# Performance work log

Measured on AMD Instinct MI355X. Metric: run time of the kernel, lower is better.

The kernel has to match this reference:

```python
import jax, jax.numpy as jnp
import numpy as np

B, M_IN, M_OUT, C = 4, 16, 32, 32


def setup_inputs() -> dict:
    key = jax.random.key(0)
    kx, = jax.random.split(key, 1)
    x = jax.random.normal(kx, (B, M_IN, C, C, C, C), dtype=jnp.float32)
    init = jnp.ones((M_IN, M_OUT), dtype=jnp.float32) / M_IN
    return {"x": x, "alpha": init, "beta": init, "gamma": init, "delta": init}


def reference(x, alpha, beta, gamma, delta):
    # Faithful to the torch code's permute+sum bookkeeping (note: torch's
    # permute(0,1,3,2,4,5).sum((2,4,5)) reduces ORIGINAL axes (3,4,5),
    # keeping original axis 2 -- identical to s1).
    s1 = x.sum(axis=(3, 4, 5))  # (B, M_in, C), keeps axis 2
    s2 = x.sum(axis=(3, 4, 5))  # same as s1 (permuted-sum in torch keeps axis 2)
    s3 = x.sum(axis=(2, 4, 5))  # keeps axis 3
    s4 = x.sum(axis=(2, 3, 5))  # keeps axis 4
    s = jnp.stack([s1, s2, s3, s4], axis=2)            # (B, M_in, 4, C)
    w = jnp.stack([alpha, beta, gamma, delta], axis=2)  # (M_in, M_out, 4)
    # 'bmic,mnd->bnic': sums over m and w's stack axis d; keeps s's stack axis i.
    out = jnp.einsum('bmic,mnd->bnic', s, w)            # (B, M_out, 4, C)
    return out
```

## Files before the change

kernel.cpp:

```cpp
#include <hip/hip_runtime.h>


__global__ __launch_bounds__(256) void zero_k(float* __restrict__ ws) {
    int i = blockIdx.x * 256 + threadIdx.x;
    if (i < 6144) ws[i] = 0.0f;
}

__global__ __launch_bounds__(256) void reduce_k(const float* __restrict__ x,
                                                float* __restrict__ ws) {
    const int t   = threadIdx.x;
    const int bid = blockIdx.x;
    const int bm  = bid >> 5;
    const int lane = t & 63;
    const int wv   = t >> 6;

    __shared__ float lds3[4][32];
    __shared__ float lds4[32];
    __shared__ float lds1[4];

    const float4* xv = (const float4*)x + (size_t)bid * 8192;

    float total = 0.0f;
    #pragma unroll
    for (int it = 0; it < 32; ++it) {
        float4 v = xv[it * 256 + t];
        float s = (v.x + v.y) + (v.z + v.w);
        total += s;
        #pragma unroll
        for (int off = 1; off < 64; off <<= 1)
            s += __shfl_xor(s, off, 64);
        if (lane == 0) lds3[wv][it] = s;
    }

    float g = total;
    g += __shfl_xor(g, 1, 64);
    g += __shfl_xor(g, 2, 64);
    g += __shfl_xor(g, 4, 64);
    if ((t & 7) == 0) lds4[t >> 3] = g;

    float wsum = g;
    wsum += __shfl_xor(wsum, 8, 64);
    wsum += __shfl_xor(wsum, 16, 64);
    wsum += __shfl_xor(wsum, 32, 64);
    if (lane == 0) lds1[wv] = wsum;

    __syncthreads();

    float* s1 = ws;
    float* s3 = ws + 2048;
    float* s4 = ws + 4096;
    if (t < 32) {
        float v3 = lds3[0][t] + lds3[1][t] + lds3[2][t] + lds3[3][t];
        atomicAdd(&s3[bm * 32 + t], v3);
        atomicAdd(&s4[bm * 32 + t], lds4[t]);
    }
    if (t == 0) {
        s1[bid] = lds1[0] + lds1[1] + lds1[2] + lds1[3];
    }
}

__global__ __launch_bounds__(256) void finalize_k(const float* __restrict__ ws,
                                                  const float* __restrict__ alpha,
                                                  const float* __restrict__ beta,
                                                  const float* __restrict__ gamma,
                                                  const float* __restrict__ delta,
                                                  float* __restrict__ out) {
    __shared__ float W[512];
    const int t = threadIdx.x;
    #pragma unroll
    for (int i = t; i < 512; i += 256)
        W[i] = alpha[i] + beta[i] + gamma[i] + delta[i];
    __syncthreads();

    int gid = blockIdx.x * 256 + t;
    int c  = gid & 31;
    int i4 = (gid >> 5) & 3;
    int n  = (gid >> 7) & 31;
    int b  = gid >> 12;

    const float* s = ws + (i4 <= 1 ? 0 : (i4 == 2 ? 2048 : 4096));
    float acc = 0.0f;
    #pragma unroll
    for (int m = 0; m < 16; ++m)
        acc += s[(b * 16 + m) * 32 + c] * W[m * 32 + n];
    out[gid] = acc;
}

extern "C" void kernel_launch(void* const* d_in, const int* in_sizes, int n_in,
                              void* d_out, int out_size, void* d_ws, size_t ws_size,
                              hipStream_t stream) {
    const float* x     = (const float*)d_in[0];
    const float* alpha = (const float*)d_in[1];
    const float* beta  = (const float*)d_in[2];
    const float* gamma = (const float*)d_in[3];
    const float* delta = (const float*)d_in[4];
    float* out = (float*)d_out;
    float* ws  = (float*)d_ws;

    zero_k<<<24, 256, 0, stream>>>(ws);
    reduce_k<<<2048, 256, 0, stream>>>(x, ws);
    finalize_k<<<64, 256, 0, stream>>>(ws, alpha, beta, gamma, delta, out);
}
```

Measured before the change: 365.7 us.

## Replace atomics with per-block partials and drop the zeroing kernel

The reduction kernel now writes per-block partial sums for the axis-3 and axis-4 reductions to separate workspace slots instead of atomically accumulating them, so the zero-init kernel launch is no longer needed. The finalize kernel sums the 32 partials per (b,m,c), stages the reduced vector in shared memory, and computes the contraction with 16 blocks. This removes one launch and the atomic contention, but the finalize step now does strided global reads over a larger workspace on only 16 blocks.

```diff
diff --git a/kernel.cpp b/kernel.cpp
--- a/kernel.cpp
+++ b/kernel.cpp
@@ -1,16 +1,13 @@
 #include <hip/hip_runtime.h>
 
 
-__global__ __launch_bounds__(256) void zero_k(float* __restrict__ ws) {
-    int i = blockIdx.x * 256 + threadIdx.x;
-    if (i < 6144) ws[i] = 0.0f;
-}
+#define P3_OFF 2048
+#define P4_OFF (2048 + 65536)
 
 __global__ __launch_bounds__(256) void reduce_k(const float* __restrict__ x,
                                                 float* __restrict__ ws) {
     const int t   = threadIdx.x;
     const int bid = blockIdx.x;
-    const int bm  = bid >> 5;
     const int lane = t & 63;
     const int wv   = t >> 6;
 
@@ -46,17 +43,13 @@
 
     __syncthreads();
 
-    float* s1 = ws;
-    float* s3 = ws + 2048;
-    float* s4 = ws + 4096;
     if (t < 32) {
         float v3 = lds3[0][t] + lds3[1][t] + lds3[2][t] + lds3[3][t];
-        atomicAdd(&s3[bm * 32 + t], v3);
-        atomicAdd(&s4[bm * 32 + t], lds4[t]);
+        ws[P3_OFF + bid * 32 + t] = v3;
+        ws[P4_OFF + bid * 32 + t] = lds4[t];
     }
-    if (t == 0) {
-        s1[bid] = lds1[0] + lds1[1] + lds1[2] + lds1[3];
-    }
+    if (t == 0)
+        ws[bid] = lds1[0] + lds1[1] + lds1[2] + lds1[3];
 }
 
 __global__ __launch_bounds__(256) void finalize_k(const float* __restrict__ ws,
@@ -66,24 +59,46 @@
                                                   const float* __restrict__ delta,
                                                   float* __restrict__ out) {
     __shared__ float W[512];
-    const int t = threadIdx.x;
+    __shared__ float S[16][32];
+    const int t  = threadIdx.x;
+    const int b  = blockIdx.x >> 2;
+    const int i4 = blockIdx.x & 3;
+
     #pragma unroll
     for (int i = t; i < 512; i += 256)
         W[i] = alpha[i] + beta[i] + gamma[i] + delta[i];
+
+    if (i4 <= 1) {
+        #pragma unroll
+        for (int i = t; i < 512; i += 256) {
+            int m = i >> 5, c = i & 31;
+            S[m][c] = ws[(b * 16 + m) * 32 + c];
+        }
+    } else {
+        const float* p = ws + (i4 == 2 ? P3_OFF : P4_OFF);
+        #pragma unroll
+        for (int i = t; i < 512; i += 256) {
+            int m = i >> 5, c = i & 31;
+            const float* q = p + (b * 16 + m) * 1024 + c;
+            float acc = 0.0f;
+            #pragma unroll
+            for (int c2 = 0; c2 < 32; ++c2)
+                acc += q[c2 * 32];
+            S[m][c] = acc;
+        }
+    }
     __syncthreads();
 
-    int gid = blockIdx.x * 256 + t;
-    int c  = gid & 31;
-    int i4 = (gid >> 5) & 3;
-    int n  = (gid >> 7) & 31;
-    int b  = gid >> 12;
-
-    const float* s = ws + (i4 <= 1 ? 0 : (i4 == 2 ? 2048 : 4096));
-    float acc = 0.0f;
     #pragma unroll
-    for (int m = 0; m < 16; ++m)
-        acc += s[(b * 16 + m) * 32 + c] * W[m * 32 + n];
-    out[gid] = acc;
+    for (int k = 0; k < 4; ++k) {
+        int idx = k * 256 + t;
+        int n = idx >> 5, c = idx & 31;
+        float acc = 0.0f;
+        #pragma unroll
+        for (int m = 0; m < 16; ++m)
+            acc += S[m][c] * W[m * 32 + n];
+        out[((b * 32 + n) * 4 + i4) * 32 + c] = acc;
+    }
 }
 
 extern "C" void kernel_launch(void* const* d_in, const int* in_sizes, int n_in,
@@ -97,7 +112,6 @@
     float* out = (float*)d_out;
     float* ws  = (float*)d_ws;
 
-    zero_k<<<24, 256, 0, stream>>>(ws);
     reduce_k<<<2048, 256, 0, stream>>>(x, ws);
-    finalize_k<<<64, 256, 0, stream>>>(ws, alpha, beta, gamma, delta, out);
+    finalize_k<<<16, 256, 0, stream>>>(ws, alpha, beta, gamma, delta, out);
 }
```

After: 365.6 us. No clear change (-0.0%).
